# Kernel optimization log

Hardware: AMD Instinct MI355X
Metric: run time of the kernel (lower is better)

## Reference

```python
import jax, jax.numpy as jnp
import numpy as np

B, S, D_IN, D_OUT, H = 4096, 128, 64, 128, 32


def setup_inputs() -> dict:
    key = jax.random.key(0)
    ks = jax.random.split(key, 8)
    x = jax.random.normal(ks[0], (B, S, D_IN), dtype=jnp.float32)
    mask = jax.random.bernoulli(ks[1], 0.7, (B, S))  # bool [B,S]
    # token-wise encoder ('net') params
    W_net = jax.random.normal(ks[2], (D_IN, D_OUT), dtype=jnp.float32) / np.sqrt(D_IN)
    b_net = jnp.zeros((D_OUT,), dtype=jnp.float32)
    # jet_to_top MLP: Linear(D_OUT,32) -> ReLU -> Linear(32,4)
    W1 = jax.random.normal(ks[3], (D_OUT, H), dtype=jnp.float32) / np.sqrt(D_OUT)
    b1 = jnp.zeros((H,), dtype=jnp.float32)
    W2 = jax.random.normal(ks[4], (H, 4), dtype=jnp.float32) / np.sqrt(H)
    b2 = jnp.zeros((4,), dtype=jnp.float32)
    return {"x": x, "W_net": W_net, "b_net": b_net,
            "W1": W1, "b1": b1, "W2": W2, "b2": b2, "mask": mask}


def reference(x, W_net, b_net, W1, b1, W2, b2, mask):
    # net: token-wise encoder -> [B, S, D_OUT]
    t_out = jnp.einsum('bsd,dh->bsh', x, W_net) + b_net

    # indices of first two valid jets per sample (stable sort pushes False last)
    idx = jnp.argsort(~mask, axis=1, stable=True)[:, :2]           # [B, 2]
    n_valid = mask.sum(axis=1)                                     # [B]

    feats = jnp.take_along_axis(t_out, idx[:, :, None], axis=1)    # [B, 2, D_OUT]

    # jet_to_top MLP on the two gathered jets
    h = jax.nn.relu(jnp.einsum('bkd,dh->bkh', feats, W1) + b1)
    preds = jnp.einsum('bkh,ho->bko', h, W2) + b2                  # [B, 2, 4]

    nv = n_valid[:, None]                                          # [B, 1]
    zero = jnp.zeros_like(preds[:, 0])
    top1 = jnp.where(nv >= 1, preds[:, 0], zero)
    top2 = jnp.where(nv >= 2, preds[:, 1], jnp.where(nv == 1, preds[:, 0], zero))
    return jnp.stack([top1, top2], axis=1)                         # [B, 2, 4]
```

## Files before the change

kernel.cpp:

```cpp
#include <hip/hip_runtime.h>

#define BATCH 4096
#define SEQ   128
#define DIN   64
#define DOUT  128
#define HID   32

__global__ __launch_bounds__(64) void fused_mlp_topk_kernel(
    const float* __restrict__ x,
    const float* __restrict__ Wn,
    const float* __restrict__ bn,
    const float* __restrict__ W1,
    const float* __restrict__ b1,
    const float* __restrict__ W2,
    const float* __restrict__ b2,
    const int*   __restrict__ mask,
    float*       __restrict__ out)
{
    const int b    = blockIdx.x;
    const int lane = threadIdx.x;

    const int m0 = mask[b * SEQ + lane];
    const int m1 = mask[b * SEQ + 64 + lane];
    const unsigned long long bal0 = __ballot(m0 != 0);
    const unsigned long long bal1 = __ballot(m1 != 0);

    int i0 = 0, i1 = 0, cnt = 0;
    if (bal0) {
        i0 = __builtin_ctzll(bal0);
        unsigned long long rem = bal0 & (bal0 - 1ull);
        if (rem)       { i1 = __builtin_ctzll(rem);       cnt = 2; }
        else if (bal1) { i1 = 64 + __builtin_ctzll(bal1); cnt = 2; }
        else           { i1 = i0;                         cnt = 1; }
    } else if (bal1) {
        i0 = 64 + __builtin_ctzll(bal1);
        unsigned long long rem = bal1 & (bal1 - 1ull);
        if (rem) { i1 = 64 + __builtin_ctzll(rem); cnt = 2; }
        else     { i1 = i0;                        cnt = 1; }
    }

    const size_t xbase = (size_t)b * SEQ * DIN;
    const float x0 = x[xbase + (size_t)i0 * DIN + lane];
    const float x1 = x[xbase + (size_t)i1 * DIN + lane];

    float f00 = bn[lane], f01 = bn[lane + 64];
    float f10 = f00,      f11 = f01;
    #pragma unroll 8
    for (int d = 0; d < DIN; ++d) {
        const float w0 = Wn[d * DOUT + lane];
        const float w1 = Wn[d * DOUT + 64 + lane];
        const float xa = __shfl(x0, d);
        const float xb = __shfl(x1, d);
        f00 = fmaf(xa, w0, f00);
        f01 = fmaf(xa, w1, f01);
        f10 = fmaf(xb, w0, f10);
        f11 = fmaf(xb, w1, f11);
    }

    __shared__ float feats[2][DOUT];
    feats[0][lane]      = f00;
    feats[0][lane + 64] = f01;
    feats[1][lane]      = f10;
    feats[1][lane + 64] = f11;
    __syncthreads();

    const int r = lane >> 5;
    const int k = lane & 31;
    float h = b1[k];
    #pragma unroll 8
    for (int j = 0; j < DOUT; ++j) {
        h = fmaf(feats[r][j], W1[j * HID + k], h);
    }
    h = fmaxf(h, 0.0f);

    __shared__ float hsm[2][HID];
    hsm[r][k] = h;
    __syncthreads();

    if (lane < 8) {
        const int rr = lane >> 2;
        const int o  = lane & 3;
        float p = b2[o];
        #pragma unroll
        for (int kk = 0; kk < HID; ++kk) {
            p = fmaf(hsm[rr][kk], W2[kk * 4 + o], p);
        }
        out[b * 8 + lane] = (cnt >= 1) ? p : 0.0f;
    }
}

extern "C" void kernel_launch(void* const* d_in, const int* in_sizes, int n_in,
                              void* d_out, int out_size, void* d_ws, size_t ws_size,
                              hipStream_t stream) {
    const float* x    = (const float*)d_in[0];
    const float* Wn   = (const float*)d_in[1];
    const float* bn   = (const float*)d_in[2];
    const float* W1   = (const float*)d_in[3];
    const float* b1   = (const float*)d_in[4];
    const float* W2   = (const float*)d_in[5];
    const float* b2   = (const float*)d_in[6];
    const int*   mask = (const int*)d_in[7];
    float* out = (float*)d_out;

    fused_mlp_topk_kernel<<<BATCH, 64, 0, stream>>>(x, Wn, bn, W1, b1, W2, b2, mask, out);
}
```

Baseline: 183.9 us.

## Pack four samples per block and vectorize the per-sample MLP loops

Each 256-thread block now processes four samples, one wave each, with per-wave LDS buffers and no block barriers. The gathered x rows are staged in LDS and read as float4 instead of broadcast by per-element shuffles. Each lane computes two adjacent outputs with float2 weight loads. The hidden and output dot products use split accumulators to shorten the FMA dependency chains. This relies on intra-wave ordering of LDS accesses without explicit synchronization.

```diff
diff --git a/kernel.cpp b/kernel.cpp
--- a/kernel.cpp
+++ b/kernel.cpp
@@ -5,8 +5,9 @@
 #define DIN   64
 #define DOUT  128
 #define HID   32
+#define WPB   4
 
-__global__ __launch_bounds__(64) void fused_mlp_topk_kernel(
+__global__ __launch_bounds__(WPB * 64) void fused_mlp_topk_kernel(
     const float* __restrict__ x,
     const float* __restrict__ Wn,
     const float* __restrict__ bn,
@@ -17,8 +18,14 @@
     const int*   __restrict__ mask,
     float*       __restrict__ out)
 {
-    const int b    = blockIdx.x;
-    const int lane = threadIdx.x;
+    const int tid  = threadIdx.x;
+    const int lane = tid & 63;
+    const int w    = tid >> 6;
+    const int b    = blockIdx.x * WPB + w;
+
+    __shared__ __align__(16) float xs[WPB][2][DIN];
+    __shared__ __align__(16) float fs[WPB][2][DOUT];
+    __shared__ __align__(16) float hs[WPB][2][HID];
 
     const int m0 = mask[b * SEQ + lane];
     const int m1 = mask[b * SEQ + 64 + lane];
@@ -40,52 +47,55 @@
     }
 
     const size_t xbase = (size_t)b * SEQ * DIN;
-    const float x0 = x[xbase + (size_t)i0 * DIN + lane];
-    const float x1 = x[xbase + (size_t)i1 * DIN + lane];
+    xs[w][0][lane] = x[xbase + (size_t)i0 * DIN + lane];
+    xs[w][1][lane] = x[xbase + (size_t)i1 * DIN + lane];
 
-    float f00 = bn[lane], f01 = bn[lane + 64];
-    float f10 = f00,      f11 = f01;
-    #pragma unroll 8
-    for (int d = 0; d < DIN; ++d) {
-        const float w0 = Wn[d * DOUT + lane];
-        const float w1 = Wn[d * DOUT + 64 + lane];
-        const float xa = __shfl(x0, d);
-        const float xb = __shfl(x1, d);
-        f00 = fmaf(xa, w0, f00);
-        f01 = fmaf(xa, w1, f01);
-        f10 = fmaf(xb, w0, f10);
-        f11 = fmaf(xb, w1, f11);
+    const int j0 = lane * 2;
+    float f00 = bn[j0], f01 = bn[j0 + 1];
+    float f10 = f00,    f11 = f01;
+    #pragma unroll
+    for (int d = 0; d < DIN; d += 4) {
+        const float4 xa = *(const float4*)&xs[w][0][d];
+        const float4 xb = *(const float4*)&xs[w][1][d];
+        const float2 wa = *(const float2*)&Wn[(d + 0) * DOUT + j0];
+        const float2 wb = *(const float2*)&Wn[(d + 1) * DOUT + j0];
+        const float2 wc = *(const float2*)&Wn[(d + 2) * DOUT + j0];
+        const float2 wd = *(const float2*)&Wn[(d + 3) * DOUT + j0];
+        f00 = fmaf(xa.x, wa.x, f00);  f01 = fmaf(xa.x, wa.y, f01);
+        f10 = fmaf(xb.x, wa.x, f10);  f11 = fmaf(xb.x, wa.y, f11);
+        f00 = fmaf(xa.y, wb.x, f00);  f01 = fmaf(xa.y, wb.y, f01);
+        f10 = fmaf(xb.y, wb.x, f10);  f11 = fmaf(xb.y, wb.y, f11);
+        f00 = fmaf(xa.z, wc.x, f00);  f01 = fmaf(xa.z, wc.y, f01);
+        f10 = fmaf(xb.z, wc.x, f10);  f11 = fmaf(xb.z, wc.y, f11);
+        f00 = fmaf(xa.w, wd.x, f00);  f01 = fmaf(xa.w, wd.y, f01);
+        f10 = fmaf(xb.w, wd.x, f10);  f11 = fmaf(xb.w, wd.y, f11);
     }
-
-    __shared__ float feats[2][DOUT];
-    feats[0][lane]      = f00;
-    feats[0][lane + 64] = f01;
-    feats[1][lane]      = f10;
-    feats[1][lane + 64] = f11;
-    __syncthreads();
+    *(float2*)&fs[w][0][j0] = make_float2(f00, f01);
+    *(float2*)&fs[w][1][j0] = make_float2(f10, f11);
 
     const int r = lane >> 5;
     const int k = lane & 31;
-    float h = b1[k];
-    #pragma unroll 8
-    for (int j = 0; j < DOUT; ++j) {
-        h = fmaf(feats[r][j], W1[j * HID + k], h);
+    float h0 = b1[k], h1 = 0.f, h2 = 0.f, h3 = 0.f;
+    #pragma unroll
+    for (int j = 0; j < DOUT; j += 4) {
+        const float4 fv = *(const float4*)&fs[w][r][j];
+        h0 = fmaf(fv.x, W1[(j + 0) * HID + k], h0);
+        h1 = fmaf(fv.y, W1[(j + 1) * HID + k], h1);
+        h2 = fmaf(fv.z, W1[(j + 2) * HID + k], h2);
+        h3 = fmaf(fv.w, W1[(j + 3) * HID + k], h3);
     }
-    h = fmaxf(h, 0.0f);
-
-    __shared__ float hsm[2][HID];
-    hsm[r][k] = h;
-    __syncthreads();
+    hs[w][r][k] = fmaxf((h0 + h1) + (h2 + h3), 0.0f);
 
     if (lane < 8) {
         const int rr = lane >> 2;
         const int o  = lane & 3;
-        float p = b2[o];
+        float p0 = b2[o], p1 = 0.f;
         #pragma unroll
-        for (int kk = 0; kk < HID; ++kk) {
-            p = fmaf(hsm[rr][kk], W2[kk * 4 + o], p);
+        for (int kk = 0; kk < HID; kk += 2) {
+            p0 = fmaf(hs[w][rr][kk + 0], W2[(kk + 0) * 4 + o], p0);
+            p1 = fmaf(hs[w][rr][kk + 1], W2[(kk + 1) * 4 + o], p1);
         }
-        out[b * 8 + lane] = (cnt >= 1) ? p : 0.0f;
+        out[b * 8 + lane] = (cnt >= 1) ? (p0 + p1) : 0.0f;
     }
 }
 
@@ -102,5 +112,6 @@
     const int*   mask = (const int*)d_in[7];
     float* out = (float*)d_out;
 
-    fused_mlp_topk_kernel<<<BATCH, 64, 0, stream>>>(x, Wn, bn, W1, b1, W2, b2, mask, out);
+    fused_mlp_topk_kernel<<<BATCH / WPB, WPB * 64, 0, stream>>>(
+        x, Wn, bn, W1, b1, W2, b2, mask, out);
 }
```

Result: no change. 184.4 us (+0.2%).
